# Kernel tuning notes

Measured on AMD Instinct MI355X. Metric: run time of the kernel, lower is better.

The kernel has to match this reference:

```python
import jax, jax.numpy as jnp
import numpy as np

N, NFEAT, NHID, E, P, STEPS = 100000, 256, 128, 3200000, 200000, 5
EPS = 1e-6


def _p(key, shape, scale=0.05):
    return (jax.random.normal(key, shape, dtype=jnp.float32) * scale)


def setup_inputs() -> dict:
    key = jax.random.key(0)
    ks = jax.random.split(key, 32)
    inp = {
        "inputs": jax.random.normal(ks[0], (N, NFEAT), dtype=jnp.float32),
        "edge_row": jnp.sort(jax.random.randint(ks[1], (E,), 0, N, dtype=jnp.int32)),
        "edge_col": jax.random.randint(ks[2], (E,), 0, N, dtype=jnp.int32),
        "edge_w": jax.random.uniform(ks[3], (E,), dtype=jnp.float32),
        "x_idx": jax.random.randint(ks[4], (P,), 0, N, dtype=jnp.int32),
        "y_idx": jax.random.randint(ks[5], (P,), 0, N, dtype=jnp.int32),
        # input gates: Linear(nfeat, nhid) with bias
        "Wr_in": _p(ks[6], (NFEAT, NHID)), "br_in": _p(ks[7], (NHID,)),
        "Wi_in": _p(ks[8], (NFEAT, NHID)), "bi_in": _p(ks[9], (NHID,)),
        "Wn_in": _p(ks[10], (NFEAT, NHID)), "bn_in": _p(ks[11], (NHID,)),
        # hidden GCN gates: weight_self + weight_neighbor, no bias
        "Hr_self": _p(ks[12], (NHID, NHID)), "Hr_nb": _p(ks[13], (NHID, NHID)),
        "Hi_self": _p(ks[14], (NHID, NHID)), "Hi_nb": _p(ks[15], (NHID, NHID)),
        "Hh_self": _p(ks[16], (NHID, NHID)), "Hh_nb": _p(ks[17], (NHID, NHID)),
        # post-GRU MLP fc1..fc3
        "W1": _p(ks[18], (NHID, NHID)), "b1": _p(ks[19], (NHID,)),
        "W2": _p(ks[20], (NHID, NHID)), "b2": _p(ks[21], (NHID,)),
        "W3": _p(ks[22], (NHID, NHID)), "b3": _p(ks[23], (NHID,)),
        # layernorm
        "gamma": jnp.ones((NHID,), jnp.float32), "beta": jnp.zeros((NHID,), jnp.float32),
        # decoder
        "Wd1": _p(ks[24], (2 * NHID, NHID)), "bd1": _p(ks[25], (NHID,)),
        "Wd2": _p(ks[26], (NHID, 1)), "bd2": _p(ks[27], (1,)),
    }
    return inp


def _spmm(row, col, w, x):
    # sparse [N,N] @ dense [N,D] via gather + segment_sum
    return jax.ops.segment_sum(x[col] * w[:, None], row, num_segments=N)


def _gcn(h, w_self, w_nb, row, col, ew):
    return h @ w_self + _spmm(row, col, ew, h @ w_nb)


def reference(inputs, edge_row, edge_col, edge_w, x_idx, y_idx,
              Wr_in, br_in, Wi_in, bi_in, Wn_in, bn_in,
              Hr_self, Hr_nb, Hi_self, Hi_nb, Hh_self, Hh_nb,
              W1, b1, W2, b2, W3, b3, gamma, beta,
              Wd1, bd1, Wd2, bd2):
    # input-gate projections are loop-invariant
    in_r = inputs @ Wr_in + br_in
    in_i = inputs @ Wi_in + bi_in
    in_n = inputs @ Wn_in + bn_in
    h = jnp.zeros((inputs.shape[0], NHID), dtype=inputs.dtype)
    for _ in range(STEPS):
        r = jax.nn.sigmoid(in_r + _gcn(h, Hr_self, Hr_nb, edge_row, edge_col, edge_w))
        i = jax.nn.sigmoid(in_i + _gcn(h, Hi_self, Hi_nb, edge_row, edge_col, edge_w))
        n = jnp.tanh(in_n + r * _gcn(h, Hh_self, Hh_nb, edge_row, edge_col, edge_w))
        h = (1.0 - i) * n + i * h
    x = jax.nn.relu(h @ W1 + b1)
    x = jax.nn.relu(x @ W2 + b2)
    x = jax.nn.relu(x @ W3 + b3)
    # torch LayerNorm variant: unbiased std, eps added to std (not var)
    mean = jnp.mean(x, axis=-1, keepdims=True)
    std = jnp.std(x, axis=-1, keepdims=True, ddof=1)
    z = gamma * (x - mean) / (std + EPS) + beta
    # MLP decoder on node pairs
    hcat = jnp.concatenate([z[x_idx], z[y_idx]], axis=1)  # [P, 2*nhid]
    d = jax.nn.relu(hcat @ Wd1 + bd1)
    d = jax.nn.sigmoid(d @ Wd2 + bd2)  # [P, 1]
    return d, z
```

## Files before the change

kernel.cpp:

```cpp
#include <hip/hip_runtime.h>
#include <hip/hip_bf16.h>

#define N_NODES 100000
#define NFEAT 256
#define NHID 128
#define NEDGE 3200000
#define NPAIR 200000
#define NSTEPS 5

typedef __attribute__((ext_vector_type(8))) short short8x;
typedef __attribute__((ext_vector_type(4))) float f32x4;

__device__ __forceinline__ float sigmoidf_(float x) {
    return 1.f / (1.f + __expf(-x));
}
__device__ __forceinline__ unsigned short f2bf_bits(float f) {
    union { float f; unsigned int u; } c; c.f = f;
    unsigned int r = (c.u + 0x7FFFu + ((c.u >> 16) & 1u)) >> 16;
    return (unsigned short)r;
}
__device__ __forceinline__ float bf_bits2f(unsigned short b) {
    union { float f; unsigned int u; } c; c.u = ((unsigned int)b) << 16;
    return c.f;
}
__device__ __forceinline__ int swz8(int row, int q) {
    return row * 32 + ((q + (row >> 1)) & 3) * 8;
}

__global__ void zero_u16(unsigned short* __restrict__ p, long long n) {
    long long i = (long long)blockIdx.x * blockDim.x + threadIdx.x;
    if (i < n) p[i] = 0;
}

__global__ void build_row_ptr(const int* __restrict__ rows, int E, int N, int* __restrict__ row_ptr) {
    int i = blockIdx.x * blockDim.x + threadIdx.x;
    if (i > N) return;
    int lo = 0, hi = E;
    while (lo < hi) {
        int mid = (lo + hi) >> 1;
        if (rows[mid] < i) lo = mid + 1; else hi = mid;
    }
    row_ptr[i] = lo;
}

__global__ void pack_kmajor(const float* __restrict__ W, int K, int NCsrc,
                            unsigned short* __restrict__ out, int NCtot, int coff, int koff) {
    int idx = blockIdx.x * blockDim.x + threadIdx.x;
    if (idx >= K * NCsrc) return;
    int k = idx / NCsrc, j = idx - k * NCsrc;
    int kg = k + koff;
    out[(size_t)(kg >> 5) * NCtot * 32 + (size_t)(coff + j) * 32 + (kg & 31)] = f2bf_bits(W[idx]);
}

__global__ void pack_bin(const float* __restrict__ br, const float* __restrict__ bi,
                         const float* __restrict__ bn, float* __restrict__ bin) {
    int i = blockIdx.x * blockDim.x + threadIdx.x;
    if (i >= 384) return;
    bin[i] = (i < 128) ? br[i] : (i < 256) ? bi[i - 128] : bn[i - 256];
}

#define SPMM_ACC(hv, we) { \
    acc[0] += (we) * bf_bits2f((unsigned short)(hv).x); \
    acc[1] += (we) * bf_bits2f((unsigned short)((hv).x >> 16)); \
    acc[2] += (we) * bf_bits2f((unsigned short)(hv).y); \
    acc[3] += (we) * bf_bits2f((unsigned short)((hv).y >> 16)); \
    acc[4] += (we) * bf_bits2f((unsigned short)(hv).z); \
    acc[5] += (we) * bf_bits2f((unsigned short)((hv).z >> 16)); \
    acc[6] += (we) * bf_bits2f((unsigned short)(hv).w); \
    acc[7] += (we) * bf_bits2f((unsigned short)((hv).w >> 16)); }

__global__ __launch_bounds__(256) void spmm_bf16_ilp(
    const int* __restrict__ row_ptr, const int* __restrict__ col,
    const float* __restrict__ w, const unsigned short* __restrict__ hbf,
    unsigned short* __restrict__ hsbf, int N)
{
    int v = blockIdx.x * 4 + (threadIdx.x >> 6);
    int lane = threadIdx.x & 63;
    int g = lane >> 4;
    int l16 = lane & 15;
    if (v >= N) return;
    int e0 = row_ptr[v], e1 = row_ptr[v + 1];
    float acc[8] = {};
    int e = e0 + g;
    for (; e + 12 < e1; e += 16) {
        int c1 = col[e], c2 = col[e + 4], c3 = col[e + 8], c4 = col[e + 12];
        float w1 = w[e], w2 = w[e + 4], w3 = w[e + 8], w4 = w[e + 12];
        const uint4 h1 = *reinterpret_cast<const uint4*>(hbf + (size_t)c1 * NHID + l16 * 8);
        const uint4 h2 = *reinterpret_cast<const uint4*>(hbf + (size_t)c2 * NHID + l16 * 8);
        const uint4 h3 = *reinterpret_cast<const uint4*>(hbf + (size_t)c3 * NHID + l16 * 8);
        const uint4 h4 = *reinterpret_cast<const uint4*>(hbf + (size_t)c4 * NHID + l16 * 8);
        SPMM_ACC(h1, w1) SPMM_ACC(h2, w2) SPMM_ACC(h3, w3) SPMM_ACC(h4, w4)
    }
    for (; e < e1; e += 4) {
        int cc = col[e];
        float we = w[e];
        const uint4 hv = *reinterpret_cast<const uint4*>(hbf + (size_t)cc * NHID + l16 * 8);
        SPMM_ACC(hv, we)
    }
    #pragma unroll
    for (int q = 0; q < 8; q++) {
        acc[q] += __shfl_xor(acc[q], 16, 64);
        acc[q] += __shfl_xor(acc[q], 32, 64);
    }
    if (g == 0) {
        uint4 o;
        o.x = (unsigned int)f2bf_bits(acc[0]) | ((unsigned int)f2bf_bits(acc[1]) << 16);
        o.y = (unsigned int)f2bf_bits(acc[2]) | ((unsigned int)f2bf_bits(acc[3]) << 16);
        o.z = (unsigned int)f2bf_bits(acc[4]) | ((unsigned int)f2bf_bits(acc[5]) << 16);
        o.w = (unsigned int)f2bf_bits(acc[6]) | ((unsigned int)f2bf_bits(acc[7]) << 16);
        *reinterpret_cast<uint4*>(hsbf + (size_t)v * NHID + l16 * 8) = o;
    }
}

__global__ __launch_bounds__(256, 2) void gate_step_mfma(
    const unsigned short* __restrict__ hsbf, unsigned short* __restrict__ hbf,
    const unsigned short* __restrict__ IN, const unsigned short* __restrict__ WBg, int M)
{
    __shared__ unsigned short As[64 * 32];
    __shared__ unsigned short Bs[384 * 32];

    const int tid = threadIdx.x;
    const int wid = tid >> 6;
    const int lane = tid & 63;
    const int row0 = blockIdx.x * 64;
    const int l15 = lane & 15;
    const int lhi = lane >> 4;

    f32x4 acc[3][2][4] = {};

    const int ar = tid >> 2;
    const int aq = tid & 3;
    const int agr = row0 + ar;

    for (int s = 0; s < 8; s++) {
        {
            short8x va = short8x(0);
            if (agr < M) {
                const unsigned short* src = (s < 4)
                    ? (hbf  + (size_t)agr * 128 + s * 32)
                    : (hsbf + (size_t)agr * 128 + (s - 4) * 32);
                va = *reinterpret_cast<const short8x*>(src + aq * 8);
            }
            *reinterpret_cast<short8x*>(&As[swz8(ar, aq)]) = va;
        }
        {
            const unsigned short* wbs = WBg + (size_t)s * 384 * 32;
            #pragma unroll
            for (int i = 0; i < 6; i++) {
                int id = tid + i * 256;
                int c = id >> 2, q = id & 3;
                short8x vb = *reinterpret_cast<const short8x*>(wbs + id * 8);
                *reinterpret_cast<short8x*>(&Bs[swz8(c, q)]) = vb;
            }
        }
        __syncthreads();

        short8x a[4];
        #pragma unroll
        for (int rb = 0; rb < 4; rb++)
            a[rb] = *reinterpret_cast<const short8x*>(&As[swz8(16 * rb + l15, lhi)]);
        #pragma unroll
        for (int p = 0; p < 3; p++) {
            #pragma unroll
            for (int cb = 0; cb < 2; cb++) {
                int c0 = 128 * p + 32 * wid + 16 * cb + l15;
                short8x b = *reinterpret_cast<const short8x*>(&Bs[swz8(c0, lhi)]);
                #pragma unroll
                for (int rb = 0; rb < 4; rb++)
                    acc[p][cb][rb] = __builtin_amdgcn_mfma_f32_16x16x32_bf16(b, a[rb], acc[p][cb][rb], 0, 0, 0);
            }
        }
        __syncthreads();
    }

    #pragma unroll
    for (int rb = 0; rb < 4; rb++) {
        int row = row0 + 16 * rb + l15;
        if (row >= M) continue;
        size_t ib = (size_t)row * 384;
        size_t ob = (size_t)row * 128;
        #pragma unroll
        for (int cb = 0; cb < 2; cb++) {
            int cq = 32 * wid + 16 * cb + 4 * lhi;
            const ushort4 vr = *reinterpret_cast<const ushort4*>(IN + ib + cq);
            const ushort4 vi = *reinterpret_cast<const ushort4*>(IN + ib + 128 + cq);
            const ushort4 vn = *reinterpret_cast<const ushort4*>(IN + ib + 256 + cq);
            const ushort4 vh = *reinterpret_cast<const ushort4*>(hbf + ob + cq);
            const unsigned short ra[4] = {vr.x, vr.y, vr.z, vr.w};
            const unsigned short ia[4] = {vi.x, vi.y, vi.z, vi.w};
            const unsigned short na[4] = {vn.x, vn.y, vn.z, vn.w};
            const unsigned short ha[4] = {vh.x, vh.y, vh.z, vh.w};
            unsigned short oa[4];
            #pragma unroll
            for (int j = 0; j < 4; j++) {
                float g_r = acc[0][cb][rb][j] + bf_bits2f(ra[j]);
                float g_i = acc[1][cb][rb][j] + bf_bits2f(ia[j]);
                float rr = sigmoidf_(g_r);
                float gi = sigmoidf_(g_i);
                float nn = tanhf(bf_bits2f(na[j]) + rr * acc[2][cb][rb][j]);
                oa[j] = f2bf_bits((1.f - gi) * nn + gi * bf_bits2f(ha[j]));
            }
            ushort4 st; st.x = oa[0]; st.y = oa[1]; st.z = oa[2]; st.w = oa[3];
            *reinterpret_cast<ushort4*>(hbf + ob + cq) = st;
        }
    }
}

template<int K, int NC, bool F32IN, bool RELU, bool BF16OUT>
__global__ __launch_bounds__(256, 2) void mfma_gemm(
    const void* __restrict__ Xv, const unsigned short* __restrict__ WBx,
    const float* __restrict__ bias, void* __restrict__ C, int M)
{
    constexpr int KS = K / 32;
    constexpr int BI = NC / 64;
    constexpr int NCW = NC / 4;
    constexpr int CB = NCW / 16;
    __shared__ unsigned short As[64 * 32];
    __shared__ unsigned short Bs[NC * 32];

    const int tid = threadIdx.x;
    const int wid = tid >> 6;
    const int lane = tid & 63;
    const int l15 = lane & 15;
    const int lhi = lane >> 4;
    const int row0 = blockIdx.x * 64;

    f32x4 acc[CB][4] = {};

    const int ar = tid >> 2;
    const int aq = tid & 3;
    const int agr = row0 + ar;

    for (int s = 0; s < KS; s++) {
        {
            short8x va = short8x(0);
            if (agr < M) {
                if (F32IN) {
                    const float* src = (const float*)Xv + (size_t)agr * K + s * 32 + aq * 8;
                    const float4 f0 = *reinterpret_cast<const float4*>(src);
                    const float4 f1 = *reinterpret_cast<const float4*>(src + 4);
                    va[0] = (short)f2bf_bits(f0.x); va[1] = (short)f2bf_bits(f0.y);
                    va[2] = (short)f2bf_bits(f0.z); va[3] = (short)f2bf_bits(f0.w);
                    va[4] = (short)f2bf_bits(f1.x); va[5] = (short)f2bf_bits(f1.y);
                    va[6] = (short)f2bf_bits(f1.z); va[7] = (short)f2bf_bits(f1.w);
                } else {
                    va = *reinterpret_cast<const short8x*>(
                        (const unsigned short*)Xv + (size_t)agr * K + s * 32 + aq * 8);
                }
            }
            *reinterpret_cast<short8x*>(&As[swz8(ar, aq)]) = va;
        }
        {
            const unsigned short* wbs = WBx + (size_t)s * NC * 32;
            #pragma unroll
            for (int i = 0; i < BI; i++) {
                int id = tid + i * 256;
                int c = id >> 2, q = id & 3;
                short8x vb = *reinterpret_cast<const short8x*>(wbs + id * 8);
                *reinterpret_cast<short8x*>(&Bs[swz8(c, q)]) = vb;
            }
        }
        __syncthreads();

        short8x a[4];
        #pragma unroll
        for (int rb = 0; rb < 4; rb++)
            a[rb] = *reinterpret_cast<const short8x*>(&As[swz8(16 * rb + l15, lhi)]);
        #pragma unroll
        for (int cb = 0; cb < CB; cb++) {
            int c0 = NCW * wid + 16 * cb + l15;
            short8x b = *reinterpret_cast<const short8x*>(&Bs[swz8(c0, lhi)]);
            #pragma unroll
            for (int rb = 0; rb < 4; rb++)
                acc[cb][rb] = __builtin_amdgcn_mfma_f32_16x16x32_bf16(b, a[rb], acc[cb][rb], 0, 0, 0);
        }
        __syncthreads();
    }

    #pragma unroll
    for (int rb = 0; rb < 4; rb++) {
        int row = row0 + 16 * rb + l15;
        if (row >= M) continue;
        #pragma unroll
        for (int cb = 0; cb < CB; cb++) {
            int cq = NCW * wid + 16 * cb + 4 * lhi;
            float4 bv = make_float4(0.f, 0.f, 0.f, 0.f);
            if (bias) bv = *reinterpret_cast<const float4*>(bias + cq);
            const float bva[4] = {bv.x, bv.y, bv.z, bv.w};
            float o[4];
            #pragma unroll
            for (int j = 0; j < 4; j++) {
                float v = acc[cb][rb][j] + bva[j];
                if (RELU) v = fmaxf(v, 0.f);
                o[j] = v;
            }
            if (BF16OUT) {
                ushort4 st;
                st.x = f2bf_bits(o[0]); st.y = f2bf_bits(o[1]);
                st.z = f2bf_bits(o[2]); st.w = f2bf_bits(o[3]);
                *reinterpret_cast<ushort4*>((unsigned short*)C + (size_t)row * NC + cq) = st;
            } else {
                float4 st; st.x = o[0]; st.y = o[1]; st.z = o[2]; st.w = o[3];
                *reinterpret_cast<float4*>((float*)C + (size_t)row * NC + cq) = st;
            }
        }
    }
}

#define XT_STRIDE 136
__global__ __launch_bounds__(256, 2) void mlp_tail(
    const unsigned short* __restrict__ hbf,
    const unsigned short* __restrict__ WB1, const unsigned short* __restrict__ WB2,
    const unsigned short* __restrict__ WB3, const unsigned short* __restrict__ WBd,
    const float* __restrict__ b1, const float* __restrict__ b2, const float* __restrict__ b3,
    const float* __restrict__ gamma, const float* __restrict__ beta,
    float* __restrict__ out_z, unsigned short* __restrict__ UV, int M)
{
    __shared__ unsigned short As[64 * 32];
    __shared__ unsigned short Bs[256 * 32];
    __shared__ unsigned short xT[64 * XT_STRIDE];

    const int tid = threadIdx.x;
    const int wid = tid >> 6;
    const int lane = tid & 63;
    const int l15 = lane & 15;
    const int lhi = lane >> 4;
    const int row0 = blockIdx.x * 64;
    const int ar = tid >> 2;
    const int aq = tid & 3;

    #pragma unroll
    for (int i = 0; i < 4; i++) {
        int id = tid + i * 256;
        int r = id >> 4, ch = id & 15;
        short8x v = short8x(0);
        if (row0 + r < M)
            v = *reinterpret_cast<const short8x*>(hbf + (size_t)(row0 + r) * 128 + ch * 8);
        *reinterpret_cast<short8x*>(&xT[r * XT_STRIDE + ch * 8]) = v;
    }
    __syncthreads();

    const unsigned short* WLs[3] = {WB1, WB2, WB3};
    const float* bLs[3] = {b1, b2, b3};
    for (int L = 0; L < 3; L++) {
        f32x4 acc[2][4] = {};
        for (int s = 0; s < 4; s++) {
            {
                short8x va = *reinterpret_cast<const short8x*>(&xT[ar * XT_STRIDE + s * 32 + aq * 8]);
                *reinterpret_cast<short8x*>(&As[swz8(ar, aq)]) = va;
            }
            {
                const unsigned short* wbs = WLs[L] + (size_t)s * 128 * 32;
                #pragma unroll
                for (int i = 0; i < 2; i++) {
                    int id = tid + i * 256;
                    int c = id >> 2, q = id & 3;
                    short8x vb = *reinterpret_cast<const short8x*>(wbs + id * 8);
                    *reinterpret_cast<short8x*>(&Bs[swz8(c, q)]) = vb;
                }
            }
            __syncthreads();
            short8x a[4];
            #pragma unroll
            for (int rb = 0; rb < 4; rb++)
                a[rb] = *reinterpret_cast<const short8x*>(&As[swz8(16 * rb + l15, lhi)]);
            #pragma unroll
            for (int cb = 0; cb < 2; cb++) {
                int c0 = 32 * wid + 16 * cb + l15;
                short8x b = *reinterpret_cast<const short8x*>(&Bs[swz8(c0, lhi)]);
                #pragma unroll
                for (int rb = 0; rb < 4; rb++)
                    acc[cb][rb] = __builtin_amdgcn_mfma_f32_16x16x32_bf16(b, a[rb], acc[cb][rb], 0, 0, 0);
            }
            __syncthreads();
        }
        #pragma unroll
        for (int rb = 0; rb < 4; rb++) {
            int r = 16 * rb + l15;
            #pragma unroll
            for (int cb = 0; cb < 2; cb++) {
                int cq = 32 * wid + 16 * cb + 4 * lhi;
                const float4 bv = *reinterpret_cast<const float4*>(bLs[L] + cq);
                const float bva[4] = {bv.x, bv.y, bv.z, bv.w};
                ushort4 st;
                unsigned short* o = (unsigned short*)&st;
                #pragma unroll
                for (int j = 0; j < 4; j++)
                    o[j] = f2bf_bits(fmaxf(acc[cb][rb][j] + bva[j], 0.f));
                *reinterpret_cast<ushort4*>(&xT[r * XT_STRIDE + cq]) = st;
            }
        }
        __syncthreads();
    }

    {
        int r = tid >> 2;
        int grp = tid & 3;
        int c0 = grp * 32;
        float xv[32];
        #pragma unroll
        for (int k = 0; k < 4; k++) {
            short8x v = *reinterpret_cast<const short8x*>(&xT[r * XT_STRIDE + c0 + k * 8]);
            #pragma unroll
            for (int j = 0; j < 8; j++) xv[k * 8 + j] = bf_bits2f((unsigned short)v[j]);
        }
        float s = 0.f;
        #pragma unroll
        for (int q = 0; q < 32; q++) s += xv[q];
        s += __shfl_xor(s, 1, 64);
        s += __shfl_xor(s, 2, 64);
        float mean = s * (1.f / 128.f);
        float vs = 0.f;
        #pragma unroll
        for (int q = 0; q < 32; q++) { float d = xv[q] - mean; vs += d * d; }
        vs += __shfl_xor(vs, 1, 64);
        vs += __shfl_xor(vs, 2, 64);
        float inv = 1.f / (sqrtf(vs / 127.f) + 1e-6f);
        int grow = row0 + r;
        #pragma unroll
        for (int k = 0; k < 4; k++) {
            const float4 gm = *reinterpret_cast<const float4*>(gamma + c0 + k * 8);
            const float4 gm2 = *reinterpret_cast<const float4*>(gamma + c0 + k * 8 + 4);
            const float4 bt = *reinterpret_cast<const float4*>(beta + c0 + k * 8);
            const float4 bt2 = *reinterpret_cast<const float4*>(beta + c0 + k * 8 + 4);
            const float gms[8] = {gm.x, gm.y, gm.z, gm.w, gm2.x, gm2.y, gm2.z, gm2.w};
            const float bts[8] = {bt.x, bt.y, bt.z, bt.w, bt2.x, bt2.y, bt2.z, bt2.w};
            float z[8];
            short8x zb;
            #pragma unroll
            for (int j = 0; j < 8; j++) {
                z[j] = gms[j] * (xv[k * 8 + j] - mean) * inv + bts[j];
                zb[j] = (short)f2bf_bits(z[j]);
            }
            *reinterpret_cast<short8x*>(&xT[r * XT_STRIDE + c0 + k * 8]) = zb;
            if (grow < M) {
                float4 z0 = make_float4(z[0], z[1], z[2], z[3]);
                float4 z1 = make_float4(z[4], z[5], z[6], z[7]);
                *reinterpret_cast<float4*>(out_z + (size_t)grow * 128 + c0 + k * 8) = z0;
                *reinterpret_cast<float4*>(out_z + (size_t)grow * 128 + c0 + k * 8 + 4) = z1;
            }
        }
    }
    __syncthreads();

    {
        f32x4 acc[4][4] = {};
        for (int s = 0; s < 4; s++) {
            {
                short8x va = *reinterpret_cast<const short8x*>(&xT[ar * XT_STRIDE + s * 32 + aq * 8]);
                *reinterpret_cast<short8x*>(&As[swz8(ar, aq)]) = va;
            }
            {
                const unsigned short* wbs = WBd + (size_t)s * 256 * 32;
                #pragma unroll
                for (int i = 0; i < 4; i++) {
                    int id = tid + i * 256;
                    int c = id >> 2, q = id & 3;
                    short8x vb = *reinterpret_cast<const short8x*>(wbs + id * 8);
                    *reinterpret_cast<short8x*>(&Bs[swz8(c, q)]) = vb;
                }
            }
            __syncthreads();
            short8x a[4];
            #pragma unroll
            for (int rb = 0; rb < 4; rb++)
                a[rb] = *reinterpret_cast<const short8x*>(&As[swz8(16 * rb + l15, lhi)]);
            #pragma unroll
            for (int cb = 0; cb < 4; cb++) {
                int c0 = 64 * wid + 16 * cb + l15;
                short8x b = *reinterpret_cast<const short8x*>(&Bs[swz8(c0, lhi)]);
                #pragma unroll
                for (int rb = 0; rb < 4; rb++)
                    acc[cb][rb] = __builtin_amdgcn_mfma_f32_16x16x32_bf16(b, a[rb], acc[cb][rb], 0, 0, 0);
            }
            __syncthreads();
        }
        #pragma unroll
        for (int rb = 0; rb < 4; rb++) {
            int row = row0 + 16 * rb + l15;
            if (row >= M) continue;
            #pragma unroll
            for (int cb = 0; cb < 4; cb++) {
                int cq = 64 * wid + 16 * cb + 4 * lhi;
                ushort4 st;
                st.x = f2bf_bits(acc[cb][rb][0]); st.y = f2bf_bits(acc[cb][rb][1]);
                st.z = f2bf_bits(acc[cb][rb][2]); st.w = f2bf_bits(acc[cb][rb][3]);
                *reinterpret_cast<ushort4*>(UV + (size_t)row * 256 + cq) = st;
            }
        }
    }
}

__global__ __launch_bounds__(256) void decoder_pairs(
    const unsigned short* __restrict__ UV,
    const int* __restrict__ xi, const int* __restrict__ yi,
    const float* __restrict__ bd1, const float* __restrict__ Wd2,
    const float* __restrict__ bd2, float* __restrict__ dout, int P)
{
    __shared__ float b1s[128], w2s[128];
    if (threadIdx.x < 128) {
        b1s[threadIdx.x] = bd1[threadIdx.x];
        w2s[threadIdx.x] = Wd2[threadIdx.x];
    }
    __syncthreads();
    int p = blockIdx.x * 256 + threadIdx.x;
    if (p >= P) return;
    const unsigned short* ur = UV + (size_t)xi[p] * 256;
    const unsigned short* vr = UV + (size_t)yi[p] * 256 + 128;
    float part = 0.f;
    #pragma unroll
    for (int j0 = 0; j0 < 128; j0 += 8) {
        const uint4 ua = *reinterpret_cast<const uint4*>(ur + j0);
        const uint4 va = *reinterpret_cast<const uint4*>(vr + j0);
        float uf[8], vf[8];
        uf[0] = bf_bits2f((unsigned short)ua.x); uf[1] = bf_bits2f((unsigned short)(ua.x >> 16));
        uf[2] = bf_bits2f((unsigned short)ua.y); uf[3] = bf_bits2f((unsigned short)(ua.y >> 16));
        uf[4] = bf_bits2f((unsigned short)ua.z); uf[5] = bf_bits2f((unsigned short)(ua.z >> 16));
        uf[6] = bf_bits2f((unsigned short)ua.w); uf[7] = bf_bits2f((unsigned short)(ua.w >> 16));
        vf[0] = bf_bits2f((unsigned short)va.x); vf[1] = bf_bits2f((unsigned short)(va.x >> 16));
        vf[2] = bf_bits2f((unsigned short)va.y); vf[3] = bf_bits2f((unsigned short)(va.y >> 16));
        vf[4] = bf_bits2f((unsigned short)va.z); vf[5] = bf_bits2f((unsigned short)(va.z >> 16));
        vf[6] = bf_bits2f((unsigned short)va.w); vf[7] = bf_bits2f((unsigned short)(va.w >> 16));
        #pragma unroll
        for (int q = 0; q < 8; q++) {
            float t = uf[q] + vf[q] + b1s[j0 + q];
            part += fmaxf(t, 0.f) * w2s[j0 + q];
        }
    }
    dout[p] = sigmoidf_(part + bd2[0]);
}

extern "C" void kernel_launch(void* const* d_in, const int* in_sizes, int n_in,
                              void* d_out, int out_size, void* d_ws, size_t ws_size,
                              hipStream_t stream) {
    const float* inputs = (const float*)d_in[0];
    const int* edge_row = (const int*)d_in[1];
    const int* edge_col = (const int*)d_in[2];
    const float* edge_w = (const float*)d_in[3];
    const int* x_idx = (const int*)d_in[4];
    const int* y_idx = (const int*)d_in[5];
    const float* Wr_in = (const float*)d_in[6];  const float* br_in = (const float*)d_in[7];
    const float* Wi_in = (const float*)d_in[8];  const float* bi_in = (const float*)d_in[9];
    const float* Wn_in = (const float*)d_in[10]; const float* bn_in = (const float*)d_in[11];
    const float* Hr_self = (const float*)d_in[12]; const float* Hr_nb = (const float*)d_in[13];
    const float* Hi_self = (const float*)d_in[14]; const float* Hi_nb = (const float*)d_in[15];
    const float* Hh_self = (const float*)d_in[16]; const float* Hh_nb = (const float*)d_in[17];
    const float* W1 = (const float*)d_in[18]; const float* b1 = (const float*)d_in[19];
    const float* W2 = (const float*)d_in[20]; const float* b2 = (const float*)d_in[21];
    const float* W3 = (const float*)d_in[22]; const float* b3 = (const float*)d_in[23];
    const float* gamma = (const float*)d_in[24]; const float* beta = (const float*)d_in[25];
    const float* Wd1 = (const float*)d_in[26]; const float* bd1 = (const float*)d_in[27];
    const float* Wd2 = (const float*)d_in[28]; const float* bd2 = (const float*)d_in[29];

    float* out_d = (float*)d_out;
    float* out_z = ((float*)d_out) + NPAIR;

    char* base = (char*)d_ws;
    size_t off = 0;
    auto take = [&](size_t bytes) { void* p = base + off; off = (off + bytes + 255) & ~(size_t)255; return p; };
    int*            row_ptr = (int*)           take((size_t)(N_NODES + 1) * 4);
    unsigned short* WBg     = (unsigned short*)take((size_t)8 * 384 * 32 * 2);
    unsigned short* WBin    = (unsigned short*)take((size_t)8 * 384 * 32 * 2);
    unsigned short* WB1     = (unsigned short*)take((size_t)4 * 128 * 32 * 2);
    unsigned short* WB2     = (unsigned short*)take((size_t)4 * 128 * 32 * 2);
    unsigned short* WB3     = (unsigned short*)take((size_t)4 * 128 * 32 * 2);
    unsigned short* WBd     = (unsigned short*)take((size_t)4 * 256 * 32 * 2);
    float*          bin     = (float*)         take(384 * 4);
    unsigned short* IN      = (unsigned short*)take((size_t)N_NODES * 384 * 2);
    unsigned short* hbf     = (unsigned short*)take((size_t)N_NODES * NHID * 2);
    unsigned short* hsbf    = (unsigned short*)take((size_t)N_NODES * NHID * 2);
    if (off > ws_size) return;

    build_row_ptr<<<(N_NODES + 256) / 256, 256, 0, stream>>>(edge_row, NEDGE, N_NODES, row_ptr);
    pack_kmajor<<<64, 256, 0, stream>>>(Hr_self, 128, 128, WBg, 384, 0, 0);
    pack_kmajor<<<64, 256, 0, stream>>>(Hi_self, 128, 128, WBg, 384, 128, 0);
    pack_kmajor<<<64, 256, 0, stream>>>(Hh_self, 128, 128, WBg, 384, 256, 0);
    pack_kmajor<<<64, 256, 0, stream>>>(Hr_nb,   128, 128, WBg, 384, 0, 128);
    pack_kmajor<<<64, 256, 0, stream>>>(Hi_nb,   128, 128, WBg, 384, 128, 128);
    pack_kmajor<<<64, 256, 0, stream>>>(Hh_nb,   128, 128, WBg, 384, 256, 128);
    pack_kmajor<<<128, 256, 0, stream>>>(Wr_in, 256, 128, WBin, 384, 0, 0);
    pack_kmajor<<<128, 256, 0, stream>>>(Wi_in, 256, 128, WBin, 384, 128, 0);
    pack_kmajor<<<128, 256, 0, stream>>>(Wn_in, 256, 128, WBin, 384, 256, 0);
    pack_kmajor<<<64, 256, 0, stream>>>(W1, 128, 128, WB1, 128, 0, 0);
    pack_kmajor<<<64, 256, 0, stream>>>(W2, 128, 128, WB2, 128, 0, 0);
    pack_kmajor<<<64, 256, 0, stream>>>(W3, 128, 128, WB3, 128, 0, 0);
    pack_kmajor<<<64, 256, 0, stream>>>(Wd1,             128, 128, WBd, 256, 0, 0);
    pack_kmajor<<<64, 256, 0, stream>>>(Wd1 + 128 * 128, 128, 128, WBd, 256, 128, 0);
    pack_bin<<<2, 256, 0, stream>>>(br_in, bi_in, bn_in, bin);
    {
        long long n = (long long)N_NODES * NHID;
        zero_u16<<<(unsigned)((n + 255) / 256), 256, 0, stream>>>(hbf, n);
    }
    int grid64 = (N_NODES + 63) / 64;
    mfma_gemm<256, 384, true, false, true><<<grid64, 256, 0, stream>>>(inputs, WBin, bin, IN, N_NODES);
    for (int s = 0; s < NSTEPS; s++) {
        spmm_bf16_ilp<<<(N_NODES + 3) / 4, 256, 0, stream>>>(row_ptr, edge_col, edge_w, hbf, hsbf, N_NODES);
        gate_step_mfma<<<grid64, 256, 0, stream>>>(hsbf, hbf, IN, WBg, N_NODES);
    }
    unsigned short* UV = IN;
    mlp_tail<<<grid64, 256, 0, stream>>>(hbf, WB1, WB2, WB3, WBd, b1, b2, b3,
                                         gamma, beta, out_z, UV, N_NODES);
    decoder_pairs<<<(NPAIR + 255) / 256, 256, 0, stream>>>(
        UV, x_idx, y_idx, bd1, Wd2, bd2, out_d, NPAIR);
}
```

Baseline: 1.085 ms.

## Fuse SpMM aggregation into gate kernel with ping-pong hidden buffers

Merges the per-step SpMM and the MFMA gate kernel into one launch. Each block aggregates neighbours for its 64 rows into shared memory, then feeds that tile straight to the MFMA loop, which skips the global round trip through hsbf. Hidden state is double-buffered so blocks can read the old h while writing the new one. The cost is that each wave now walks 16 rows in sequence, and the kernel uses more shared memory, which lowers occupancy and memory-level parallelism for the latency-bound gather.

After: 1.576 ms. 45.2% more time.

```diff
diff --git a/kernel.cpp b/kernel.cpp
--- a/kernel.cpp
+++ b/kernel.cpp
@@ -69,55 +69,16 @@
     acc[6] += (we) * bf_bits2f((unsigned short)(hv).w); \
     acc[7] += (we) * bf_bits2f((unsigned short)((hv).w >> 16)); }
 
-__global__ __launch_bounds__(256) void spmm_bf16_ilp(
+#define HS_STRIDE 136
+__global__ __launch_bounds__(256, 2) void spmm_gate_fused(
     const int* __restrict__ row_ptr, const int* __restrict__ col,
-    const float* __restrict__ w, const unsigned short* __restrict__ hbf,
-    unsigned short* __restrict__ hsbf, int N)
-{
-    int v = blockIdx.x * 4 + (threadIdx.x >> 6);
-    int lane = threadIdx.x & 63;
-    int g = lane >> 4;
-    int l16 = lane & 15;
-    if (v >= N) return;
-    int e0 = row_ptr[v], e1 = row_ptr[v + 1];
-    float acc[8] = {};
-    int e = e0 + g;
-    for (; e + 12 < e1; e += 16) {
-        int c1 = col[e], c2 = col[e + 4], c3 = col[e + 8], c4 = col[e + 12];
-        float w1 = w[e], w2 = w[e + 4], w3 = w[e + 8], w4 = w[e + 12];
-        const uint4 h1 = *reinterpret_cast<const uint4*>(hbf + (size_t)c1 * NHID + l16 * 8);
-        const uint4 h2 = *reinterpret_cast<const uint4*>(hbf + (size_t)c2 * NHID + l16 * 8);
-        const uint4 h3 = *reinterpret_cast<const uint4*>(hbf + (size_t)c3 * NHID + l16 * 8);
-        const uint4 h4 = *reinterpret_cast<const uint4*>(hbf + (size_t)c4 * NHID + l16 * 8);
-        SPMM_ACC(h1, w1) SPMM_ACC(h2, w2) SPMM_ACC(h3, w3) SPMM_ACC(h4, w4)
-    }
-    for (; e < e1; e += 4) {
-        int cc = col[e];
-        float we = w[e];
-        const uint4 hv = *reinterpret_cast<const uint4*>(hbf + (size_t)cc * NHID + l16 * 8);
-        SPMM_ACC(hv, we)
-    }
-    #pragma unroll
-    for (int q = 0; q < 8; q++) {
-        acc[q] += __shfl_xor(acc[q], 16, 64);
-        acc[q] += __shfl_xor(acc[q], 32, 64);
-    }
-    if (g == 0) {
-        uint4 o;
-        o.x = (unsigned int)f2bf_bits(acc[0]) | ((unsigned int)f2bf_bits(acc[1]) << 16);
-        o.y = (unsigned int)f2bf_bits(acc[2]) | ((unsigned int)f2bf_bits(acc[3]) << 16);
-        o.z = (unsigned int)f2bf_bits(acc[4]) | ((unsigned int)f2bf_bits(acc[5]) << 16);
-        o.w = (unsigned int)f2bf_bits(acc[6]) | ((unsigned int)f2bf_bits(acc[7]) << 16);
-        *reinterpret_cast<uint4*>(hsbf + (size_t)v * NHID + l16 * 8) = o;
-    }
-}
-
-__global__ __launch_bounds__(256, 2) void gate_step_mfma(
-    const unsigned short* __restrict__ hsbf, unsigned short* __restrict__ hbf,
+    const float* __restrict__ w,
+    const unsigned short* __restrict__ hold, unsigned short* __restrict__ hnew,
     const unsigned short* __restrict__ IN, const unsigned short* __restrict__ WBg, int M)
 {
     __shared__ unsigned short As[64 * 32];
     __shared__ unsigned short Bs[384 * 32];
+    __shared__ unsigned short hsT[64 * HS_STRIDE];
 
     const int tid = threadIdx.x;
     const int wid = tid >> 6;
@@ -126,21 +87,57 @@
     const int l15 = lane & 15;
     const int lhi = lane >> 4;
 
+    {
+        const int g = lane >> 4;
+        const int l16 = lane & 15;
+        for (int rr = 0; rr < 16; rr++) {
+            int lr = wid * 16 + rr;
+            int v = row0 + lr;
+            float acc[8] = {};
+            if (v < M) {
+                int e0 = row_ptr[v], e1 = row_ptr[v + 1];
+                int e = e0 + g;
+                for (; e + 12 < e1; e += 16) {
+                    int c1 = col[e], c2 = col[e + 4], c3 = col[e + 8], c4 = col[e + 12];
+                    float w1 = w[e], w2 = w[e + 4], w3 = w[e + 8], w4 = w[e + 12];
+                    const uint4 h1 = *reinterpret_cast<const uint4*>(hold + (size_t)c1 * NHID + l16 * 8);
+                    const uint4 h2 = *reinterpret_cast<const uint4*>(hold + (size_t)c2 * NHID + l16 * 8);
+                    const uint4 h3 = *reinterpret_cast<const uint4*>(hold + (size_t)c3 * NHID + l16 * 8);
+                    const uint4 h4 = *reinterpret_cast<const uint4*>(hold + (size_t)c4 * NHID + l16 * 8);
+                    SPMM_ACC(h1, w1) SPMM_ACC(h2, w2) SPMM_ACC(h3, w3) SPMM_ACC(h4, w4)
+                }
+                for (; e < e1; e += 4) {
+                    int cc = col[e];
+                    float we = w[e];
+                    const uint4 hv = *reinterpret_cast<const uint4*>(hold + (size_t)cc * NHID + l16 * 8);
+                    SPMM_ACC(hv, we)
+                }
+            }
+            #pragma unroll
+            for (int q = 0; q < 8; q++) {
+                acc[q] += __shfl_xor(acc[q], 16, 64);
+                acc[q] += __shfl_xor(acc[q], 32, 64);
+            }
+            if (g == 0) {
+                short8x o;
+                #pragma unroll
+                for (int q = 0; q < 8; q++) o[q] = (short)f2bf_bits(acc[q]);
+                *reinterpret_cast<short8x*>(&hsT[lr * HS_STRIDE + l16 * 8]) = o;
+            }
+        }
+    }
+    __syncthreads();
+
     f32x4 acc[3][2][4] = {};
-
     const int ar = tid >> 2;
     const int aq = tid & 3;
     const int agr = row0 + ar;
 
     for (int s = 0; s < 8; s++) {
-        {
+        if (s < 4) {
             short8x va = short8x(0);
-            if (agr < M) {
-                const unsigned short* src = (s < 4)
-                    ? (hbf  + (size_t)agr * 128 + s * 32)
-                    : (hsbf + (size_t)agr * 128 + (s - 4) * 32);
-                va = *reinterpret_cast<const short8x*>(src + aq * 8);
-            }
+            if (agr < M)
+                va = *reinterpret_cast<const short8x*>(hold + (size_t)agr * 128 + s * 32 + aq * 8);
             *reinterpret_cast<short8x*>(&As[swz8(ar, aq)]) = va;
         }
         {
@@ -156,9 +153,16 @@
         __syncthreads();
 
         short8x a[4];
-        #pragma unroll
-        for (int rb = 0; rb < 4; rb++)
-            a[rb] = *reinterpret_cast<const short8x*>(&As[swz8(16 * rb + l15, lhi)]);
+        if (s < 4) {
+            #pragma unroll
+            for (int rb = 0; rb < 4; rb++)
+                a[rb] = *reinterpret_cast<const short8x*>(&As[swz8(16 * rb + l15, lhi)]);
+        } else {
+            #pragma unroll
+            for (int rb = 0; rb < 4; rb++)
+                a[rb] = *reinterpret_cast<const short8x*>(
+                    &hsT[(16 * rb + l15) * HS_STRIDE + (s - 4) * 32 + lhi * 8]);
+        }
         #pragma unroll
         for (int p = 0; p < 3; p++) {
             #pragma unroll
@@ -185,7 +189,7 @@
             const ushort4 vr = *reinterpret_cast<const ushort4*>(IN + ib + cq);
             const ushort4 vi = *reinterpret_cast<const ushort4*>(IN + ib + 128 + cq);
             const ushort4 vn = *reinterpret_cast<const ushort4*>(IN + ib + 256 + cq);
-            const ushort4 vh = *reinterpret_cast<const ushort4*>(hbf + ob + cq);
+            const ushort4 vh = *reinterpret_cast<const ushort4*>(hold + ob + cq);
             const unsigned short ra[4] = {vr.x, vr.y, vr.z, vr.w};
             const unsigned short ia[4] = {vi.x, vi.y, vi.z, vi.w};
             const unsigned short na[4] = {vn.x, vn.y, vn.z, vn.w};
@@ -201,7 +205,7 @@
                 oa[j] = f2bf_bits((1.f - gi) * nn + gi * bf_bits2f(ha[j]));
             }
             ushort4 st; st.x = oa[0]; st.y = oa[1]; st.z = oa[2]; st.w = oa[3];
-            *reinterpret_cast<ushort4*>(hbf + ob + cq) = st;
+            *reinterpret_cast<ushort4*>(hnew + ob + cq) = st;
         }
     }
 }
@@ -567,8 +571,8 @@
     unsigned short* WBd     = (unsigned short*)take((size_t)4 * 256 * 32 * 2);
     float*          bin     = (float*)         take(384 * 4);
     unsigned short* IN      = (unsigned short*)take((size_t)N_NODES * 384 * 2);
-    unsigned short* hbf     = (unsigned short*)take((size_t)N_NODES * NHID * 2);
-    unsigned short* hsbf    = (unsigned short*)take((size_t)N_NODES * NHID * 2);
+    unsigned short* hb0     = (unsigned short*)take((size_t)N_NODES * NHID * 2);
+    unsigned short* hb1     = (unsigned short*)take((size_t)N_NODES * NHID * 2);
     if (off > ws_size) return;
 
     build_row_ptr<<<(N_NODES + 256) / 256, 256, 0, stream>>>(edge_row, NEDGE, N_NODES, row_ptr);
@@ -589,16 +593,19 @@
     pack_bin<<<2, 256, 0, stream>>>(br_in, bi_in, bn_in, bin);
     {
         long long n = (long long)N_NODES * NHID;
-        zero_u16<<<(unsigned)((n + 255) / 256), 256, 0, stream>>>(hbf, n);
+        zero_u16<<<(unsigned)((n + 255) / 256), 256, 0, stream>>>(hb0, n);
     }
     int grid64 = (N_NODES + 63) / 64;
     mfma_gemm<256, 384, true, false, true><<<grid64, 256, 0, stream>>>(inputs, WBin, bin, IN, N_NODES);
+    unsigned short* hcur = hb0;
+    unsigned short* hnxt = hb1;
     for (int s = 0; s < NSTEPS; s++) {
-        spmm_bf16_ilp<<<(N_NODES + 3) / 4, 256, 0, stream>>>(row_ptr, edge_col, edge_w, hbf, hsbf, N_NODES);
-        gate_step_mfma<<<grid64, 256, 0, stream>>>(hsbf, hbf, IN, WBg, N_NODES);
+        spmm_gate_fused<<<grid64, 256, 0, stream>>>(row_ptr, edge_col, edge_w,
+                                                    hcur, hnxt, IN, WBg, N_NODES);
+        unsigned short* t = hcur; hcur = hnxt; hnxt = t;
     }
     unsigned short* UV = IN;
-    mlp_tail<<<grid64, 256, 0, stream>>>(hbf, WB1, WB2, WB3, WBd, b1, b2, b3,
+    mlp_tail<<<grid64, 256, 0, stream>>>(hcur, WB1, WB2, WB3, WBd, b1, b2, b3,
                                          gamma, beta, out_z, UV, N_NODES);
     decoder_pairs<<<(NPAIR + 255) / 256, 256, 0, stream>>>(
         UV, x_idx, y_idx, bd1, Wd2, bd2, out_d, NPAIR);
```
